# Kernel tuning notes

Hardware: AMD Instinct MI355X
Metric: run time of the kernel (lower is better)

The kernel has to match this reference:

```python
import jax, jax.numpy as jnp
import numpy as np

E, H, I, T = 8, 1024, 4096, 8192  # experts, hidden, intermediate, total tokens


def setup_inputs() -> dict:
    key = jax.random.key(0)
    k1, k2, k3 = jax.random.split(key, 3)
    hiddens = jax.random.normal(k1, (T, H), dtype=jnp.float32)
    # expert weights, scaled like standard init
    w1_weight = jax.random.normal(k2, (E, H, I), dtype=jnp.float32) * (1.0 / np.sqrt(H).astype(np.float32))
    w2_weight = jax.random.normal(k3, (E, I, H), dtype=jnp.float32) * (1.0 / np.sqrt(I).astype(np.float32))
    # tokens are pre-grouped by expert; equal load of T//E tokens per expert
    batch_sizes = jnp.full((E,), T // E, dtype=jnp.int32)
    return {"hiddens": hiddens, "batch_sizes": batch_sizes,
            "w1_weight": w1_weight, "w2_weight": w2_weight}


def _gmm(x, w, batch_sizes):
    """Grouped matmul: rows of x are grouped contiguously by expert.
    x: [T, K], w: [E, K, N], batch_sizes: [E] (sums to T). Returns [T, N].
    Loop is over the small fixed expert count; each iteration is a dense
    GEMM with rows outside the expert's segment masked to zero.
    """
    n_experts = w.shape[0]
    ends = jnp.cumsum(batch_sizes)
    starts = ends - batch_sizes
    tok = jnp.arange(x.shape[0])[:, None]  # [T, 1]
    out = jnp.zeros((x.shape[0], w.shape[2]), dtype=x.dtype)
    for e in range(n_experts):
        mask = (tok >= starts[e]) & (tok < ends[e])  # [T, 1]
        out = out + jnp.where(mask, x, jnp.zeros((), x.dtype)) @ w[e]
    return out


def reference(hiddens, batch_sizes, w1_weight, w2_weight):
    up = _gmm(hiddens, w1_weight, batch_sizes)    # [T, I]
    down = _gmm(up, w2_weight, batch_sizes)       # [T, H]
    return down
```

## Files before the change

### kernel.cpp

```cpp
#include <hip/hip_runtime.h>
#include <hip/hip_bf16.h>


typedef unsigned short u16;
typedef unsigned int u32;
typedef __attribute__((ext_vector_type(8))) short bf16x8;
typedef __attribute__((ext_vector_type(4))) float f32x4;
typedef __attribute__((ext_vector_type(4))) u32 u32x4;

#define E_N 8
#define H_N 1024
#define I_N 4096
#define T_N 8192

#define GLD2LDS16(g, l)                                                        \
  __builtin_amdgcn_global_load_lds(                                            \
      (const __attribute__((address_space(1))) void*)(g),                      \
      (__attribute__((address_space(3))) void*)(l), 16, 0, 0)

__device__ __forceinline__ u32 pkbf(float lo, float hi) {
  u32 a = __float_as_uint(lo) + 0x8000u;
  u32 b = __float_as_uint(hi) + 0x8000u;
  return __builtin_amdgcn_perm(b, a, 0x07060302u);
}

__device__ __forceinline__ u16 f2bf(float f) {
  __hip_bfloat16 h = __float2bfloat16(f);
  return *(reinterpret_cast<u16*>(&h));
}

__global__ __launch_bounds__(256) void cvt_kernel(const float* __restrict__ src,
                                                  u16* __restrict__ dst) {
  const size_t i = ((size_t)blockIdx.x * 256 + threadIdx.x) * 8;
  float4 a = *(const float4*)(src + i);
  float4 b = *(const float4*)(src + i + 4);
  *(u32x4*)(dst + i) = (u32x4){pkbf(a.x, a.y), pkbf(a.z, a.w),
                               pkbf(b.x, b.y), pkbf(b.z, b.w)};
}

__global__ __launch_bounds__(256) void transp_kernel(const float* __restrict__ w2,
                                                     u16* __restrict__ w2t) {
  __shared__ float tile[64 * 65];
  const int tid = threadIdx.x;
  const int h0 = blockIdx.x * 64;
  const int i0 = blockIdx.y * 64;
  const float* src = w2 + (size_t)blockIdx.z * I_N * H_N;
  u16* dst = w2t + (size_t)blockIdx.z * H_N * I_N;

  {
    const int r = tid >> 4;
    const int c4 = (tid & 15) * 4;
#pragma unroll
    for (int rr = 0; rr < 4; rr++) {
      const int row = rr * 16 + r;
      float4 v = *(const float4*)(src + (size_t)(i0 + row) * H_N + h0 + c4);
      tile[row * 65 + c4 + 0] = v.x;
      tile[row * 65 + c4 + 1] = v.y;
      tile[row * 65 + c4 + 2] = v.z;
      tile[row * 65 + c4 + 3] = v.w;
    }
  }
  __syncthreads();

  {
    const int hr = tid >> 3;
    const int ic = (tid & 7) * 8;
#pragma unroll
    for (int hh = 0; hh < 2; hh++) {
      const int h = hh * 32 + hr;
      u32 p[4];
#pragma unroll
      for (int j = 0; j < 4; j++)
        p[j] = pkbf(tile[(ic + 2 * j) * 65 + h], tile[(ic + 2 * j + 1) * 65 + h]);
      *(u32x4*)(dst + (size_t)(h0 + h) * I_N + i0 + ic) =
          (u32x4){p[0], p[1], p[2], p[3]};
    }
  }
}

__global__ __launch_bounds__(256) void wgemm_kernel(const u16* __restrict__ w2t,
                                                    const u16* __restrict__ w1b,
                                                    u16* __restrict__ mt) {
  __shared__ u16 ldsA[4096];
  __shared__ u16 ldsB[4096];

  const int tid = threadIdx.x;
  const int lane = tid & 63;
  const int wv = tid >> 6;
  const int wm = wv >> 1, wn = wv & 1;
  const int lm = lane & 15, quad = lane >> 4;

  const int e = blockIdx.x >> 6;
  const int t = blockIdx.x & 63;
  const int row0 = (t >> 3) * 128;
  const int col0 = (t & 7) * 128;

  const u16* Ae = w2t + (size_t)e * H_N * I_N;
  const u16* Be = w1b + (size_t)e * H_N * I_N;
  u16* mte = mt + (size_t)e * H_N * H_N;

  const int s_r = tid >> 2;
  const int s_k = (tid & 3) * 8;
  const u16* gA0 = Ae + (size_t)(row0 + s_r) * I_N + s_k;
  const u16* gA1 = gA0 + (size_t)64 * I_N;
  const u16* gB0 = Be + (size_t)(col0 + s_r) * I_N + s_k;
  const u16* gB1 = gB0 + (size_t)64 * I_N;
  u16* ldsA_dst = ldsA + wv * 512;
  u16* ldsB_dst = ldsB + wv * 512;

  f32x4 acc[4][4];
#pragma unroll
  for (int i = 0; i < 4; i++)
#pragma unroll
    for (int j = 0; j < 4; j++) acc[i][j] = (f32x4){0.f, 0.f, 0.f, 0.f};

  for (int k0 = 0; k0 < I_N; k0 += 32) {
    GLD2LDS16(gA0 + k0, ldsA_dst);
    GLD2LDS16(gA1 + k0, ldsA_dst + 2048);
    GLD2LDS16(gB0 + k0, ldsB_dst);
    GLD2LDS16(gB1 + k0, ldsB_dst + 2048);

    __syncthreads();

    bf16x8 af[4], bfr[4];
#pragma unroll
    for (int mi = 0; mi < 4; mi++)
      af[mi] = *(const bf16x8*)(ldsA + (wm * 64 + mi * 16 + lm) * 32 + quad * 8);
#pragma unroll
    for (int ni = 0; ni < 4; ni++)
      bfr[ni] = *(const bf16x8*)(ldsB + (wn * 64 + ni * 16 + lm) * 32 + quad * 8);
#pragma unroll
    for (int mi = 0; mi < 4; mi++)
#pragma unroll
      for (int ni = 0; ni < 4; ni++)
        acc[mi][ni] = __builtin_amdgcn_mfma_f32_16x16x32_bf16(
            af[mi], bfr[ni], acc[mi][ni], 0, 0, 0);

    __syncthreads();
  }

  const int orow = row0 + wm * 64 + quad * 4;
  const int ocol = col0 + wn * 64 + lm;
#pragma unroll
  for (int mi = 0; mi < 4; mi++)
#pragma unroll
    for (int ni = 0; ni < 4; ni++)
#pragma unroll
      for (int r = 0; r < 4; r++)
        mte[(size_t)(orow + mi * 16 + r) * H_N + ocol + ni * 16] =
            f2bf(acc[mi][ni][r]);
}

__global__ __launch_bounds__(256) void tgemm_kernel(const u16* __restrict__ xb,
                                                    const int* __restrict__ bsz,
                                                    const u16* __restrict__ mt,
                                                    float* __restrict__ out) {
  __shared__ u16 ldsA[4096];
  __shared__ u16 ldsB[4096];

  const int tid = threadIdx.x;
  const int lane = tid & 63;
  const int wv = tid >> 6;
  const int wm = wv >> 1, wn = wv & 1;
  const int lm = lane & 15, quad = lane >> 4;

  const int bm = blockIdx.x >> 3, bn = blockIdx.x & 7;
  const int row0 = bm * 128;
  const int col0 = bn * 128;

  int e = 0, start = 0;
#pragma unroll
  for (int i = 0; i < E_N; i++) {
    int b = bsz[i];
    if (row0 >= start + b) { start += b; e = i + 1; }
  }
  const u16* mte = mt + (size_t)e * H_N * H_N;

  const int s_r = tid >> 2;
  const int s_k = (tid & 3) * 8;
  const u16* gA0 = xb + (size_t)(row0 + s_r) * H_N + s_k;
  const u16* gA1 = gA0 + (size_t)64 * H_N;
  const u16* gB0 = mte + (size_t)(col0 + s_r) * H_N + s_k;
  const u16* gB1 = gB0 + (size_t)64 * H_N;
  u16* ldsA_dst = ldsA + wv * 512;
  u16* ldsB_dst = ldsB + wv * 512;

  f32x4 acc[4][4];
#pragma unroll
  for (int i = 0; i < 4; i++)
#pragma unroll
    for (int j = 0; j < 4; j++) acc[i][j] = (f32x4){0.f, 0.f, 0.f, 0.f};

  for (int k0 = 0; k0 < H_N; k0 += 32) {
    GLD2LDS16(gA0 + k0, ldsA_dst);
    GLD2LDS16(gA1 + k0, ldsA_dst + 2048);
    GLD2LDS16(gB0 + k0, ldsB_dst);
    GLD2LDS16(gB1 + k0, ldsB_dst + 2048);

    __syncthreads();

    bf16x8 af[4], bfr[4];
#pragma unroll
    for (int mi = 0; mi < 4; mi++)
      af[mi] = *(const bf16x8*)(ldsA + (wm * 64 + mi * 16 + lm) * 32 + quad * 8);
#pragma unroll
    for (int ni = 0; ni < 4; ni++)
      bfr[ni] = *(const bf16x8*)(ldsB + (wn * 64 + ni * 16 + lm) * 32 + quad * 8);
#pragma unroll
    for (int mi = 0; mi < 4; mi++)
#pragma unroll
      for (int ni = 0; ni < 4; ni++)
        acc[mi][ni] = __builtin_amdgcn_mfma_f32_16x16x32_bf16(
            af[mi], bfr[ni], acc[mi][ni], 0, 0, 0);

    __syncthreads();
  }

  const int orow = row0 + wm * 64 + quad * 4;
  const int ocol = col0 + wn * 64 + lm;
#pragma unroll
  for (int mi = 0; mi < 4; mi++)
#pragma unroll
    for (int ni = 0; ni < 4; ni++)
#pragma unroll
      for (int r = 0; r < 4; r++)
        out[(size_t)(orow + mi * 16 + r) * H_N + ocol + ni * 16] =
            acc[mi][ni][r];
}

extern "C" void kernel_launch(void* const* d_in, const int* in_sizes, int n_in,
                              void* d_out, int out_size, void* d_ws,
                              size_t ws_size, hipStream_t stream) {
  (void)in_sizes; (void)n_in; (void)out_size; (void)ws_size;
  const float* hiddens = (const float*)d_in[0];
  const int* bsz = (const int*)d_in[1];
  const float* w1 = (const float*)d_in[2];
  const float* w2 = (const float*)d_in[3];
  float* out = (float*)d_out;

  char* ws = (char*)d_ws;
  u16* w1b = (u16*)(ws);
  u16* w2t = (u16*)(ws + (size_t)64 * 1024 * 1024);
  u16* xb  = (u16*)(ws + (size_t)128 * 1024 * 1024);
  u16* mt  = (u16*)(ws + (size_t)144 * 1024 * 1024);

  cvt_kernel<<<dim3(16384), 256, 0, stream>>>(w1, w1b);
  cvt_kernel<<<dim3(4096), 256, 0, stream>>>(hiddens, xb);
  transp_kernel<<<dim3(16, 64, E_N), 256, 0, stream>>>(w2, w2t);

  wgemm_kernel<<<dim3(512), 256, 0, stream>>>(w2t, w1b, mt);
  tgemm_kernel<<<dim3(512), 256, 0, stream>>>(xb, bsz, mt, out);
}
```

Baseline: 482.7 us.

## Split-K the weight-product GEMM and halve token GEMM row tile

The expert weight-product GEMM is split into two K halves, writing fp32 partials that a new reduce kernel sums and packs to bf16, doubling the block count. The token GEMM tile is reduced from 128 to 64 rows for more blocks. The aim is better CU occupancy on long serial K loops. This adds extra global traffic for partials, and the split path only activates when the workspace is large enough.

```diff
diff --git a/kernel.cpp b/kernel.cpp
--- a/kernel.cpp
+++ b/kernel.cpp
@@ -151,10 +151,9 @@
             f2bf(acc[mi][ni][r]);
 }
 
-__global__ __launch_bounds__(256) void tgemm_kernel(const u16* __restrict__ xb,
-                                                    const int* __restrict__ bsz,
-                                                    const u16* __restrict__ mt,
-                                                    float* __restrict__ out) {
+__global__ __launch_bounds__(256) void wgemm_split_kernel(
+    const u16* __restrict__ w2t, const u16* __restrict__ w1b,
+    float* __restrict__ mtp) {
   __shared__ u16 ldsA[4096];
   __shared__ u16 ldsB[4096];
 
@@ -164,8 +163,99 @@
   const int wm = wv >> 1, wn = wv & 1;
   const int lm = lane & 15, quad = lane >> 4;
 
+  const int kh = blockIdx.x >> 9;
+  const int bi = blockIdx.x & 511;
+  const int e = bi >> 6;
+  const int t = bi & 63;
+  const int row0 = (t >> 3) * 128;
+  const int col0 = (t & 7) * 128;
+
+  const u16* Ae = w2t + (size_t)e * H_N * I_N;
+  const u16* Be = w1b + (size_t)e * H_N * I_N;
+
+  const int s_r = tid >> 2;
+  const int s_k = (tid & 3) * 8;
+  const u16* gA0 = Ae + (size_t)(row0 + s_r) * I_N + s_k;
+  const u16* gA1 = gA0 + (size_t)64 * I_N;
+  const u16* gB0 = Be + (size_t)(col0 + s_r) * I_N + s_k;
+  const u16* gB1 = gB0 + (size_t)64 * I_N;
+  u16* ldsA_dst = ldsA + wv * 512;
+  u16* ldsB_dst = ldsB + wv * 512;
+
+  f32x4 acc[4][4];
+#pragma unroll
+  for (int i = 0; i < 4; i++)
+#pragma unroll
+    for (int j = 0; j < 4; j++) acc[i][j] = (f32x4){0.f, 0.f, 0.f, 0.f};
+
+  const int kbeg = kh * (I_N / 2);
+  for (int k0 = kbeg; k0 < kbeg + I_N / 2; k0 += 32) {
+    GLD2LDS16(gA0 + k0, ldsA_dst);
+    GLD2LDS16(gA1 + k0, ldsA_dst + 2048);
+    GLD2LDS16(gB0 + k0, ldsB_dst);
+    GLD2LDS16(gB1 + k0, ldsB_dst + 2048);
+
+    __syncthreads();
+
+    bf16x8 af[4], bfr[4];
+#pragma unroll
+    for (int mi = 0; mi < 4; mi++)
+      af[mi] = *(const bf16x8*)(ldsA + (wm * 64 + mi * 16 + lm) * 32 + quad * 8);
+#pragma unroll
+    for (int ni = 0; ni < 4; ni++)
+      bfr[ni] = *(const bf16x8*)(ldsB + (wn * 64 + ni * 16 + lm) * 32 + quad * 8);
+#pragma unroll
+    for (int mi = 0; mi < 4; mi++)
+#pragma unroll
+      for (int ni = 0; ni < 4; ni++)
+        acc[mi][ni] = __builtin_amdgcn_mfma_f32_16x16x32_bf16(
+            af[mi], bfr[ni], acc[mi][ni], 0, 0, 0);
+
+    __syncthreads();
+  }
+
+  float* dst = mtp + ((size_t)(kh * E_N + e)) * H_N * H_N;
+  const int orow = row0 + wm * 64 + quad * 4;
+  const int ocol = col0 + wn * 64 + lm;
+#pragma unroll
+  for (int mi = 0; mi < 4; mi++)
+#pragma unroll
+    for (int ni = 0; ni < 4; ni++)
+#pragma unroll
+      for (int r = 0; r < 4; r++)
+        dst[(size_t)(orow + mi * 16 + r) * H_N + ocol + ni * 16] =
+            acc[mi][ni][r];
+}
+
+__global__ __launch_bounds__(256) void reduce_mt_kernel(
+    const float* __restrict__ mtp, u16* __restrict__ mt) {
+  const size_t i = ((size_t)blockIdx.x * 256 + threadIdx.x) * 8;
+  const float* p0 = mtp + i;
+  const float* p1 = mtp + (size_t)E_N * H_N * H_N + i;
+  float4 a0 = *(const float4*)p0;
+  float4 a1 = *(const float4*)(p0 + 4);
+  float4 b0 = *(const float4*)p1;
+  float4 b1 = *(const float4*)(p1 + 4);
+  *(u32x4*)(mt + i) =
+      (u32x4){pkbf(a0.x + b0.x, a0.y + b0.y), pkbf(a0.z + b0.z, a0.w + b0.w),
+              pkbf(a1.x + b1.x, a1.y + b1.y), pkbf(a1.z + b1.z, a1.w + b1.w)};
+}
+
+__global__ __launch_bounds__(256) void tgemm_kernel(const u16* __restrict__ xb,
+                                                    const int* __restrict__ bsz,
+                                                    const u16* __restrict__ mt,
+                                                    float* __restrict__ out) {
+  __shared__ u16 ldsA[2048];
+  __shared__ u16 ldsB[4096];
+
+  const int tid = threadIdx.x;
+  const int lane = tid & 63;
+  const int wv = tid >> 6;
+  const int wm = wv >> 1, wn = wv & 1;
+  const int lm = lane & 15, quad = lane >> 4;
+
   const int bm = blockIdx.x >> 3, bn = blockIdx.x & 7;
-  const int row0 = bm * 128;
+  const int row0 = bm * 64;
   const int col0 = bn * 128;
 
   int e = 0, start = 0;
@@ -179,35 +269,33 @@
   const int s_r = tid >> 2;
   const int s_k = (tid & 3) * 8;
   const u16* gA0 = xb + (size_t)(row0 + s_r) * H_N + s_k;
-  const u16* gA1 = gA0 + (size_t)64 * H_N;
   const u16* gB0 = mte + (size_t)(col0 + s_r) * H_N + s_k;
   const u16* gB1 = gB0 + (size_t)64 * H_N;
   u16* ldsA_dst = ldsA + wv * 512;
   u16* ldsB_dst = ldsB + wv * 512;
 
-  f32x4 acc[4][4];
-#pragma unroll
-  for (int i = 0; i < 4; i++)
+  f32x4 acc[2][4];
+#pragma unroll
+  for (int i = 0; i < 2; i++)
 #pragma unroll
     for (int j = 0; j < 4; j++) acc[i][j] = (f32x4){0.f, 0.f, 0.f, 0.f};
 
   for (int k0 = 0; k0 < H_N; k0 += 32) {
     GLD2LDS16(gA0 + k0, ldsA_dst);
-    GLD2LDS16(gA1 + k0, ldsA_dst + 2048);
     GLD2LDS16(gB0 + k0, ldsB_dst);
     GLD2LDS16(gB1 + k0, ldsB_dst + 2048);
 
     __syncthreads();
 
-    bf16x8 af[4], bfr[4];
-#pragma unroll
-    for (int mi = 0; mi < 4; mi++)
-      af[mi] = *(const bf16x8*)(ldsA + (wm * 64 + mi * 16 + lm) * 32 + quad * 8);
+    bf16x8 af[2], bfr[4];
+#pragma unroll
+    for (int mi = 0; mi < 2; mi++)
+      af[mi] = *(const bf16x8*)(ldsA + (wm * 32 + mi * 16 + lm) * 32 + quad * 8);
 #pragma unroll
     for (int ni = 0; ni < 4; ni++)
       bfr[ni] = *(const bf16x8*)(ldsB + (wn * 64 + ni * 16 + lm) * 32 + quad * 8);
 #pragma unroll
-    for (int mi = 0; mi < 4; mi++)
+    for (int mi = 0; mi < 2; mi++)
 #pragma unroll
       for (int ni = 0; ni < 4; ni++)
         acc[mi][ni] = __builtin_amdgcn_mfma_f32_16x16x32_bf16(
@@ -216,10 +304,10 @@
     __syncthreads();
   }
 
-  const int orow = row0 + wm * 64 + quad * 4;
+  const int orow = row0 + wm * 32 + quad * 4;
   const int ocol = col0 + wn * 64 + lm;
 #pragma unroll
-  for (int mi = 0; mi < 4; mi++)
+  for (int mi = 0; mi < 2; mi++)
 #pragma unroll
     for (int ni = 0; ni < 4; ni++)
 #pragma unroll
@@ -231,7 +319,7 @@
 extern "C" void kernel_launch(void* const* d_in, const int* in_sizes, int n_in,
                               void* d_out, int out_size, void* d_ws,
                               size_t ws_size, hipStream_t stream) {
-  (void)in_sizes; (void)n_in; (void)out_size; (void)ws_size;
+  (void)in_sizes; (void)n_in; (void)out_size;
   const float* hiddens = (const float*)d_in[0];
   const int* bsz = (const int*)d_in[1];
   const float* w1 = (const float*)d_in[2];
@@ -243,11 +331,19 @@
   u16* w2t = (u16*)(ws + (size_t)64 * 1024 * 1024);
   u16* xb  = (u16*)(ws + (size_t)128 * 1024 * 1024);
   u16* mt  = (u16*)(ws + (size_t)144 * 1024 * 1024);
+  float* mtp = (float*)(ws + (size_t)160 * 1024 * 1024);
+  const bool splitw = ws_size >= (size_t)224 * 1024 * 1024;
 
   cvt_kernel<<<dim3(16384), 256, 0, stream>>>(w1, w1b);
   cvt_kernel<<<dim3(4096), 256, 0, stream>>>(hiddens, xb);
   transp_kernel<<<dim3(16, 64, E_N), 256, 0, stream>>>(w2, w2t);
 
-  wgemm_kernel<<<dim3(512), 256, 0, stream>>>(w2t, w1b, mt);
-  tgemm_kernel<<<dim3(512), 256, 0, stream>>>(xb, bsz, mt, out);
-}
+  if (splitw) {
+    wgemm_split_kernel<<<dim3(1024), 256, 0, stream>>>(w2t, w1b, mtp);
+    reduce_mt_kernel<<<dim3(4096), 256, 0, stream>>>(mtp, mt);
+  } else {
+    wgemm_kernel<<<dim3(512), 256, 0, stream>>>(w2t, w1b, mt);
+  }
+
+  tgemm_kernel<<<dim3(1024), 256, 0, stream>>>(xb, bsz, mt, out);
+}
```

Result: slower. 496.6 us (+2.9%).
